# Optimization experiments

Hardware: AMD Instinct MI355X
Metric: run time of the kernel (lower is better)

Reference implementation:

```python
import jax, jax.numpy as jnp
import numpy as np

NUM_HOSTS = 13


def gcn_conv_max(x, src, dst, n, W, b):
    """PyG GCNConv with aggr='max': x@W, gcn_norm (self-loops + sym norm), max-scatter, +bias.
    src/dst already include self-loop edges."""
    xw = x @ W  # [N, out]
    deg = jnp.zeros((n,), xw.dtype).at[dst].add(1.0)
    dinv = jax.lax.rsqrt(deg)  # deg >= 1 thanks to self-loops
    norm = dinv[src] * dinv[dst]  # [E+N]
    msg = norm[:, None] * xw[src]  # [E+N, out] -- the big gather
    agg = jax.ops.segment_max(msg, dst, num_segments=n)
    return agg + b


def self_attn(v, g, aW, ab, fW, fb, gW, gb):
    """SimpleSelfAttention: softmax over feature dim, weighted-sum over nodes, residual global update."""
    att = jax.nn.softmax(v @ aW + ab, axis=-1)  # [B, Nh, h]
    feat = v @ fW + fb                            # [B, Nh, h]
    out = jnp.sum(att * feat, axis=1)             # [B, h]
    g_ = jnp.concatenate([out, g], axis=-1) @ gW + gb
    return g + g_


def setup_inputs() -> dict:
    key = jax.random.key(0)
    ks = jax.random.split(key, 24)
    IN, H1, H2 = 64, 256, 64
    B, NPG = 256, 200
    N = B * NPG
    E = 409600

    x = jax.random.normal(ks[0], (N, IN), jnp.float32)
    host_idx = (jnp.arange(B)[:, None] * NPG + jnp.arange(NUM_HOSTS)[None, :]).reshape(-1).astype(jnp.int32)
    x = x.at[host_idx, 0].set(1.0)  # hosts = x[:,0]==1
    ei = jax.random.randint(ks[1], (2, E), 0, N, dtype=jnp.int64)

    def lin(k, i, o):
        k1, k2 = jax.random.split(k)
        s = 1.0 / np.sqrt(i)
        return (jax.random.uniform(k1, (i, o), jnp.float32, -s, s),
                jax.random.uniform(k2, (o,), jnp.float32, -s, s))

    W1, b1 = lin(ks[2], IN, H1)
    W2, b2 = lin(ks[3], H1, H2)
    # g0: in=IN, h=H1, g=H1 ; g1: in=H1, h=H1 ; g2: in=H2, h=H2
    a0W, a0b = lin(ks[4], IN, H1); f0W, f0b = lin(ks[5], IN, H1); g0W, g0b = lin(ks[6], H1 + H1, H1)
    a1W, a1b = lin(ks[7], H1, H1); f1W, f1b = lin(ks[8], H1, H1); g1W, g1b = lin(ks[9], H1 + H1, H1)
    a2W, a2b = lin(ks[10], H2, H2); f2W, f2b = lin(ks[11], H2, H2); g2W, g2b = lin(ks[12], H2 + H1, H1)
    o1W, o1b = lin(ks[13], H1, H2)
    o2W, o2b = lin(ks[14], H2, 1)

    return dict(x=x, ei=ei, host_idx=host_idx,
                W1=W1, b1=b1, W2=W2, b2=b2,
                a0W=a0W, a0b=a0b, f0W=f0W, f0b=f0b, g0W=g0W, g0b=g0b,
                a1W=a1W, a1b=a1b, f1W=f1W, f1b=f1b, g1W=g1W, g1b=g1b,
                a2W=a2W, a2b=a2b, f2W=f2W, f2b=f2b, g2W=g2W, g2b=g2b,
                o1W=o1W, o1b=o1b, o2W=o2W, o2b=o2b)


def reference(x, ei, host_idx,
              W1, b1, W2, b2,
              a0W, a0b, f0W, f0b, g0W, g0b,
              a1W, a1b, f1W, f1b, g1W, g1b,
              a2W, a2b, f2W, f2b, g2W, g2b,
              o1W, o1b, o2W, o2b):
    n = x.shape[0]
    B = host_idx.shape[0] // NUM_HOSTS
    loops = jnp.arange(n, dtype=ei.dtype)
    src = jnp.concatenate([ei[0], loops])
    dst = jnp.concatenate([ei[1], loops])

    hx = x[host_idx].reshape(B, NUM_HOSTS, -1)
    g = self_attn(hx, jnp.zeros((B, g0b.shape[0]), x.dtype), a0W, a0b, f0W, f0b, g0W, g0b)

    x1 = jax.nn.relu(gcn_conv_max(x, src, dst, n, W1, b1))
    g = self_attn(x1[host_idx].reshape(B, NUM_HOSTS, -1), g, a1W, a1b, f1W, f1b, g1W, g1b)

    x2 = jax.nn.relu(gcn_conv_max(x1, src, dst, n, W2, b2))
    g = self_attn(x2[host_idx].reshape(B, NUM_HOSTS, -1), g, a2W, a2b, f2W, f2b, g2W, g2b)

    return jax.nn.relu(g @ o1W + o1b) @ o2W + o2b  # [B, 1]
```

## Files before the change

### kernel.cpp

```cpp
#include <hip/hip_runtime.h>
#include <math.h>
#include <stdio.h>

#define N_NODES 51200
#define N_EDGES 409600
#define B_GRAPH 256
#define NH 13

typedef float v4f __attribute__((ext_vector_type(4)));
__device__ __forceinline__ void nt_store_f4(float* p, float4 v) {
    v4f w; w.x = v.x; w.y = v.y; w.z = v.z; w.w = v.w;
    __builtin_nontemporal_store(w, (v4f*)p);
}

__device__ __forceinline__ unsigned pack_bf2(float a, float b) {
    unsigned ua = __float_as_uint(a);
    ua = (ua + 0x7fffu + ((ua >> 16) & 1u)) >> 16;
    unsigned ub = __float_as_uint(b);
    ub = (ub + 0x7fffu + ((ub >> 16) & 1u)) & 0xffff0000u;
    return ua | ub;
}
__device__ __forceinline__ float bf_lo(unsigned u) { return __uint_as_float(u << 16); }
__device__ __forceinline__ float bf_hi(unsigned u) { return __uint_as_float(u & 0xffff0000u); }

__device__ __forceinline__ bool ei_is_64(const int* __restrict__ ei32) {
    int z = 1;
    #pragma unroll
    for (int k = 1; k < 16; k += 2) z &= (ei32[k] == 0);
    return z != 0;
}

__global__ void count_deg(const int* __restrict__ ei32, const long long* __restrict__ ei64,
                          int* __restrict__ degc) {
    int e = blockIdx.x * 256 + threadIdx.x;
    if (e >= N_EDGES) return;
    int v = ei_is_64(ei32) ? (int)ei64[N_EDGES + e] : ei32[N_EDGES + e];
    atomicAdd(&degc[v], 1);
}

__global__ void scan_block_sums(const int* __restrict__ degc, int* __restrict__ bsums) {
    __shared__ int sdata[256];
    int i = blockIdx.x * 256 + threadIdx.x;
    sdata[threadIdx.x] = degc[i];
    __syncthreads();
    for (int s = 128; s > 0; s >>= 1) {
        if (threadIdx.x < s) sdata[threadIdx.x] += sdata[threadIdx.x + s];
        __syncthreads();
    }
    if (threadIdx.x == 0) bsums[blockIdx.x] = sdata[0];
}

__global__ void scan_finalize(int* __restrict__ degc, int* __restrict__ offs,
                              float* __restrict__ dinv, const int* __restrict__ bsums) {
    __shared__ int bs[256];
    __shared__ int s[256];
    const int t = threadIdx.x;
    bs[t] = (t < 200) ? bsums[t] : 0;
    __syncthreads();
    for (int off = 1; off < 256; off <<= 1) {
        int u = (t >= off) ? bs[t - off] : 0;
        __syncthreads();
        bs[t] += u;
        __syncthreads();
    }
    int i = blockIdx.x * 256 + t;
    int cnt = degc[i];
    s[t] = cnt;
    __syncthreads();
    for (int off = 1; off < 256; off <<= 1) {
        int u = (t >= off) ? s[t - off] : 0;
        __syncthreads();
        s[t] += u;
        __syncthreads();
    }
    int base = (blockIdx.x == 0) ? 0 : bs[blockIdx.x - 1];
    int excl = base + s[t] - cnt;
    offs[i] = excl;
    dinv[i] = rsqrtf((float)(cnt + 1));
    degc[i] = excl;
    if (i == N_NODES - 1) offs[N_NODES] = N_EDGES;
}

template <int K, int WS, int YS, bool GATHER, bool SCALE, bool BIAS, bool BF16OUT>
__device__ __forceinline__ void gemm_body(const float* __restrict__ X,
        const float* __restrict__ W, const float* __restrict__ bias,
        const float* __restrict__ dinv, float* __restrict__ Y,
        int row0, const int* __restrict__ rows,
        float* __restrict__ xs, float* __restrict__ ws) {
    constexpr int BK = 32;
    constexpr int XS = BK + 4;
    const int t = threadIdx.x;
    const int ct = t & 15;
    const int rt = t >> 4;
    float acc[4][4] = {{0.f}};
    for (int kc = 0; kc < K; kc += BK) {
        __syncthreads();
        #pragma unroll
        for (int i = 0; i < 2; ++i) {
            int idx = t + i * 256;
            int q = idx & 7, r = idx >> 3;
            int xr = GATHER ? rows[r] : (row0 + r);
            float4 v = *(const float4*)(X + (size_t)xr * K + kc + q * 4);
            *(float4*)&xs[r * XS + q * 4] = v;
        }
        #pragma unroll
        for (int i = 0; i < 2; ++i) {
            int idx = t + i * 256;
            int q = idx & 15, k = idx >> 4;
            float4 v = *(const float4*)(W + (size_t)(kc + k) * WS + q * 4);
            *(float4*)&ws[k * 64 + q * 4] = v;
        }
        __syncthreads();
        #pragma unroll
        for (int kb = 0; kb < BK; kb += 4) {
            float4 wv[4];
            #pragma unroll
            for (int kk = 0; kk < 4; ++kk)
                wv[kk] = *(const float4*)&ws[(kb + kk) * 64 + ct * 4];
            #pragma unroll
            for (int r = 0; r < 4; ++r) {
                float4 xv = *(const float4*)&xs[(rt * 4 + r) * XS + kb];
                acc[r][0] = fmaf(xv.x, wv[0].x, acc[r][0]);
                acc[r][1] = fmaf(xv.x, wv[0].y, acc[r][1]);
                acc[r][2] = fmaf(xv.x, wv[0].z, acc[r][2]);
                acc[r][3] = fmaf(xv.x, wv[0].w, acc[r][3]);
                acc[r][0] = fmaf(xv.y, wv[1].x, acc[r][0]);
                acc[r][1] = fmaf(xv.y, wv[1].y, acc[r][1]);
                acc[r][2] = fmaf(xv.y, wv[1].z, acc[r][2]);
                acc[r][3] = fmaf(xv.y, wv[1].w, acc[r][3]);
                acc[r][0] = fmaf(xv.z, wv[2].x, acc[r][0]);
                acc[r][1] = fmaf(xv.z, wv[2].y, acc[r][1]);
                acc[r][2] = fmaf(xv.z, wv[2].z, acc[r][2]);
                acc[r][3] = fmaf(xv.z, wv[2].w, acc[r][3]);
                acc[r][0] = fmaf(xv.w, wv[3].x, acc[r][0]);
                acc[r][1] = fmaf(xv.w, wv[3].y, acc[r][1]);
                acc[r][2] = fmaf(xv.w, wv[3].z, acc[r][2]);
                acc[r][3] = fmaf(xv.w, wv[3].w, acc[r][3]);
            }
        }
    }
    #pragma unroll
    for (int r = 0; r < 4; ++r) {
        int row = row0 + rt * 4 + r;
        float4 o = make_float4(acc[r][0], acc[r][1], acc[r][2], acc[r][3]);
        if (BIAS) {
            o.x += bias[ct * 4 + 0];
            o.y += bias[ct * 4 + 1];
            o.z += bias[ct * 4 + 2];
            o.w += bias[ct * 4 + 3];
        }
        if (SCALE) {
            float sc = dinv[row];
            o.x *= sc; o.y *= sc; o.z *= sc; o.w *= sc;
        }
        if (BF16OUT) {
            unsigned short* yb = (unsigned short*)Y + (size_t)row * YS;
            uint2 pk;
            pk.x = pack_bf2(o.x, o.y);
            pk.y = pack_bf2(o.z, o.w);
            ((uint2*)yb)[ct] = pk;
        } else {
            *(float4*)&Y[(size_t)row * YS + ct * 4] = o;
        }
    }
}

template <int K, int NTOT, int NA_BLK, int NF_BLK, bool BF16Y>
__global__ __launch_bounds__(256) void fused_gemm(const float* __restrict__ X,
        const float* __restrict__ W, float* __restrict__ Y,
        const float* __restrict__ dinv,
        const int* __restrict__ ei32, const long long* __restrict__ ei64,
        int* __restrict__ cursor, int* __restrict__ csr,
        const float* __restrict__ XA, const int* __restrict__ host_idx,
        const float* __restrict__ aW, const float* __restrict__ ab,
        const float* __restrict__ fW, const float* __restrict__ fb,
        float* __restrict__ AF) {
    __shared__ float xs[64 * 36];
    __shared__ float ws[32 * 64];
    __shared__ int rows[64];
    const int bid = blockIdx.x;
    const int t = threadIdx.x;
    if (bid < NA_BLK) {
        const int rb = bid >> 3;
        const int cb = bid & 7;
        const int c0 = cb * 64;
        const float* Wp = (c0 < 256) ? (aW + c0) : (fW + (c0 - 256));
        const float* bp = (c0 < 256) ? (ab + c0) : (fb + (c0 - 256));
        if (t < 64) rows[t] = host_idx[rb * 64 + t];
        gemm_body<K, 256, 512, true, false, true, false>(
            XA, Wp, bp, nullptr, AF + c0, rb * 64, rows, xs, ws);
    } else if (bid < NA_BLK + NF_BLK) {
        int e = (bid - NA_BLK) * 256 + t;
        if (e < N_EDGES) {
            int u, v;
            if (ei_is_64(ei32)) { u = (int)ei64[e]; v = (int)ei64[N_EDGES + e]; }
            else                { u = ei32[e];      v = ei32[N_EDGES + e]; }
            int pos = atomicAdd(&cursor[v], 1);
            csr[pos] = u;
        }
    } else {
        const int gbid = bid - NA_BLK - NF_BLK;
        constexpr int nColBlk = NTOT / 64;
        const int rb = gbid / nColBlk;
        const int cb = gbid - rb * nColBlk;
        float* Yp = BF16Y ? (Y + cb * 32) : (Y + cb * 64);
        gemm_body<K, NTOT, NTOT, false, true, false, BF16Y>(
            X, W + cb * 64, nullptr, dinv, Yp, rb * 64, nullptr, xs, ws);
    }
}

__device__ __forceinline__ void attn_red256(const float* __restrict__ AF,
        const float* __restrict__ gW, const float* __restrict__ gb,
        const float* __restrict__ g_in, float* __restrict__ g_out, int b,
        float (*At)[256], float* red_m, float* red_s, float* cat) {
    const int t = threadIdx.x;
    const int wave = t >> 6, lane = t & 63;
    float accA[NH], accF[NH];
    #pragma unroll
    for (int j = 0; j < NH; ++j) {
        const float* r = AF + (size_t)(b * NH + j) * 512;
        accA[j] = r[t];
        accF[j] = r[256 + t];
        At[j][t] = accA[j];
    }
    __syncthreads();
    for (int j = wave; j < NH; j += 4) {
        float m = -3.402823466e38f;
        #pragma unroll
        for (int q = 0; q < 4; ++q) m = fmaxf(m, At[j][q * 64 + lane]);
        #pragma unroll
        for (int off = 32; off; off >>= 1) m = fmaxf(m, __shfl_xor(m, off));
        if (lane == 0) red_m[j] = m;
    }
    __syncthreads();
    #pragma unroll
    for (int j = 0; j < NH; ++j) At[j][t] = expf(accA[j] - red_m[j]);
    __syncthreads();
    for (int j = wave; j < NH; j += 4) {
        float s = 0.f;
        #pragma unroll
        for (int q = 0; q < 4; ++q) s += At[j][q * 64 + lane];
        #pragma unroll
        for (int off = 32; off; off >>= 1) s += __shfl_xor(s, off);
        if (lane == 0) red_s[j] = s;
    }
    __syncthreads();
    float outc = 0.f;
    #pragma unroll
    for (int j = 0; j < NH; ++j) outc += At[j][t] / red_s[j] * accF[j];
    cat[t] = outc;
    float gv = g_in ? g_in[b * 256 + t] : 0.f;
    cat[256 + t] = gv;
    __syncthreads();
    float acc = gb[t];
    const float* gwp = gW + t;
    #pragma unroll 4
    for (int i4 = 0; i4 < 128; ++i4) {
        float4 cq = ((const float4*)cat)[i4];
        const float* gw4 = gwp + (size_t)i4 * 4 * 256;
        acc = fmaf(cq.x, gw4[0], acc);
        acc = fmaf(cq.y, gw4[256], acc);
        acc = fmaf(cq.z, gw4[512], acc);
        acc = fmaf(cq.w, gw4[768], acc);
    }
    g_out[b * 256 + t] = gv + acc;
}

__global__ __launch_bounds__(256) void fused_agg256(const uint2* __restrict__ xwb,
        const float* __restrict__ dinv, const int* __restrict__ offs,
        const int* __restrict__ csr, const float* __restrict__ bias,
        float* __restrict__ out,
        const float* __restrict__ AF, const float* __restrict__ gW,
        const float* __restrict__ gb, const float* __restrict__ g_in,
        float* __restrict__ g_out) {
    __shared__ float At[NH][256];
    __shared__ float red_m[NH];
    __shared__ float red_s[NH];
    __shared__ float cat[512];
    const int bid = blockIdx.x;
    if (bid < 256) {
        attn_red256(AF, gW, gb, g_in, g_out, bid, At, red_m, red_s, cat);
        return;
    }
    int gid = (bid - 256) * 256 + threadIdx.x;
    int v = gid >> 6;
    int lane = gid & 63;
    uint2 sw = xwb[(size_t)v * 64 + lane];
    float4 acc = make_float4(bf_lo(sw.x), bf_hi(sw.x), bf_lo(sw.y), bf_hi(sw.y));
    int e0 = offs[v];
    int e1 = offs[v + 1];
    int em = e0 + ((e1 - e0) & ~7);
    for (int e = e0; e < em; e += 8) {
        int u[8];
        #pragma unroll
        for (int i = 0; i < 8; ++i) u[i] = csr[e + i];
        uint2 m[8];
        #pragma unroll
        for (int i = 0; i < 8; ++i) m[i] = xwb[(size_t)u[i] * 64 + lane];
        #pragma unroll
        for (int i = 0; i < 8; ++i) {
            acc.x = fmaxf(acc.x, bf_lo(m[i].x));
            acc.y = fmaxf(acc.y, bf_hi(m[i].x));
            acc.z = fmaxf(acc.z, bf_lo(m[i].y));
            acc.w = fmaxf(acc.w, bf_hi(m[i].y));
        }
    }
    if (em < e1) {
        int u[8];
        #pragma unroll
        for (int i = 0; i < 8; ++i) u[i] = csr[(em + i < e1) ? (em + i) : (e1 - 1)];
        uint2 m[8];
        #pragma unroll
        for (int i = 0; i < 8; ++i) m[i] = xwb[(size_t)u[i] * 64 + lane];
        #pragma unroll
        for (int i = 0; i < 8; ++i) {
            if (em + i < e1) {
                acc.x = fmaxf(acc.x, bf_lo(m[i].x));
                acc.y = fmaxf(acc.y, bf_hi(m[i].x));
                acc.z = fmaxf(acc.z, bf_lo(m[i].y));
                acc.w = fmaxf(acc.w, bf_hi(m[i].y));
            }
        }
    }
    float dv = dinv[v];
    float4 b4 = ((const float4*)bias)[lane];
    float4 o;
    o.x = fmaxf(fmaf(acc.x, dv, b4.x), 0.f);
    o.y = fmaxf(fmaf(acc.y, dv, b4.y), 0.f);
    o.z = fmaxf(fmaf(acc.z, dv, b4.z), 0.f);
    o.w = fmaxf(fmaf(acc.w, dv, b4.w), 0.f);
    nt_store_f4(out + (size_t)v * 256 + lane * 4, o);
}

__global__ __launch_bounds__(1024) void attn_graph_head(
        const float* __restrict__ AF,
        const float* __restrict__ g1W, const float* __restrict__ g1b,
        const float* __restrict__ g_in,
        const float* __restrict__ xw2,
        const float* __restrict__ dinv, const int* __restrict__ offs,
        const int* __restrict__ csr, const float* __restrict__ b2,
        const int* __restrict__ host_idx,
        const float* __restrict__ a2W, const float* __restrict__ a2b,
        const float* __restrict__ f2W, const float* __restrict__ f2b,
        const float* __restrict__ g2W, const float* __restrict__ g2b,
        const float* __restrict__ o1W, const float* __restrict__ o1b,
        const float* __restrict__ o2W, const float* __restrict__ o2b,
        float* __restrict__ out) {
    __shared__ float At[NH][256];
    __shared__ float Ft[NH][256];
    __shared__ float red_m[NH];
    __shared__ float red_s[NH];
    __shared__ float cat[512];
    __shared__ float catB[320];
    __shared__ float g1s[256];
    __shared__ float x2l[NH][64];
    __shared__ float part4[4][256];
    __shared__ float part16[16][64];
    __shared__ float grow[256];
    const int b = blockIdx.x;
    const int t = threadIdx.x;
    const int wave = t >> 6;
    const int lane = t & 63;
    const int c = t & 255;
    const int quad = t >> 8;

    if (wave < NH) {
        int hv = host_idx[b * NH + wave];
        float acc = xw2[(size_t)hv * 64 + lane];
        int e0 = offs[hv], e1 = offs[hv + 1];
        for (int e = e0; e < e1; e += 8) {
            int u[8];
            #pragma unroll
            for (int i = 0; i < 8; ++i) u[i] = csr[(e + i < e1) ? (e + i) : (e1 - 1)];
            float m[8];
            #pragma unroll
            for (int i = 0; i < 8; ++i) m[i] = xw2[(size_t)u[i] * 64 + lane];
            #pragma unroll
            for (int i = 0; i < 8; ++i)
                if (e + i < e1) acc = fmaxf(acc, m[i]);
        }
        x2l[wave][lane] = fmaxf(fmaf(acc, dinv[hv], b2[lane]), 0.f);
    }
    for (int idx = t; idx < NH * 128; idx += 1024) {
        int j = idx >> 7, q = idx & 127;
        float4 v = ((const float4*)(AF + (size_t)(b * NH + j) * 512))[q];
        if (q < 64) *(float4*)&At[j][q * 4] = v;
        else        *(float4*)&Ft[j][(q - 64) * 4] = v;
    }
    __syncthreads();
    if (wave < NH) {
        float m = -3.402823466e38f;
        #pragma unroll
        for (int q = 0; q < 4; ++q) m = fmaxf(m, At[wave][q * 64 + lane]);
        #pragma unroll
        for (int off = 32; off; off >>= 1) m = fmaxf(m, __shfl_xor(m, off));
        if (lane == 0) red_m[wave] = m;
    }
    __syncthreads();
    for (int idx = t; idx < NH * 256; idx += 1024) {
        int j = idx >> 8, cc = idx & 255;
        At[j][cc] = expf(At[j][cc] - red_m[j]);
    }
    __syncthreads();
    if (wave < NH) {
        float s = 0.f;
        #pragma unroll
        for (int q = 0; q < 4; ++q) s += At[wave][q * 64 + lane];
        #pragma unroll
        for (int off = 32; off; off >>= 1) s += __shfl_xor(s, off);
        if (lane == 0) red_s[wave] = s;
    }
    __syncthreads();
    if (quad == 0) {
        float outc = 0.f;
        #pragma unroll
        for (int j = 0; j < NH; ++j) outc += At[j][c] / red_s[j] * Ft[j][c];
        cat[c] = outc;
        cat[256 + c] = g_in[b * 256 + c];
    }
    __syncthreads();
    {
        float acc = 0.f;
        const float* gwp = g1W + c;
        #pragma unroll 4
        for (int i4 = quad * 32; i4 < quad * 32 + 32; ++i4) {
            float4 cq = ((const float4*)cat)[i4];
            const float* gw4 = gwp + (size_t)i4 * 1024;
            acc = fmaf(cq.x, gw4[0], acc);
            acc = fmaf(cq.y, gw4[256], acc);
            acc = fmaf(cq.z, gw4[512], acc);
            acc = fmaf(cq.w, gw4[768], acc);
        }
        part4[quad][c] = acc;
    }
    __syncthreads();
    if (quad == 0)
        g1s[c] = cat[256 + c] + g1b[c] +
                 part4[0][c] + part4[1][c] + part4[2][c] + part4[3][c];
    __syncthreads();
    if (wave < NH) {
        float aA = a2b[lane], aF = f2b[lane];
        #pragma unroll 8
        for (int k = 0; k < 64; ++k) {
            float xv = x2l[wave][k];
            aA = fmaf(xv, a2W[k * 64 + lane], aA);
            aF = fmaf(xv, f2W[k * 64 + lane], aF);
        }
        float m = aA;
        #pragma unroll
        for (int off = 32; off; off >>= 1) m = fmaxf(m, __shfl_xor(m, off));
        float pexp = expf(aA - m);
        float s = pexp;
        #pragma unroll
        for (int off = 32; off; off >>= 1) s += __shfl_xor(s, off);
        At[wave][lane] = pexp / s * aF;
    }
    __syncthreads();
    if (t < 64) {
        float o = 0.f;
        #pragma unroll
        for (int j = 0; j < NH; ++j) o += At[j][t];
        catB[t] = o;
    }
    if (quad == 0) catB[64 + c] = g1s[c];
    __syncthreads();
    {
        float acc = 0.f;
        const float* gwp = g2W + c;
        #pragma unroll 4
        for (int i4 = quad * 20; i4 < quad * 20 + 20; ++i4) {
            float4 cq = ((const float4*)catB)[i4];
            const float* gw4 = gwp + (size_t)i4 * 1024;
            acc = fmaf(cq.x, gw4[0], acc);
            acc = fmaf(cq.y, gw4[256], acc);
            acc = fmaf(cq.z, gw4[512], acc);
            acc = fmaf(cq.w, gw4[768], acc);
        }
        part4[quad][c] = acc;
    }
    __syncthreads();
    if (quad == 0)
        grow[c] = g1s[c] + g2b[c] +
                  part4[0][c] + part4[1][c] + part4[2][c] + part4[3][c];
    __syncthreads();
    {
        float hp = 0.f;
        #pragma unroll
        for (int k = wave * 16; k < wave * 16 + 16; ++k)
            hp = fmaf(grow[k], o1W[(size_t)k * 64 + lane], hp);
        part16[wave][lane] = hp;
    }
    __syncthreads();
    if (wave == 0) {
        float h = o1b[lane];
        #pragma unroll
        for (int w = 0; w < 16; ++w) h += part16[w][lane];
        h = fmaxf(h, 0.f);
        float sres = h * o2W[lane];
        #pragma unroll
        for (int off = 32; off; off >>= 1) sres += __shfl_xor(sres, off);
        if (lane == 0) out[b] = sres + o2b[0];
    }
}

extern "C" void kernel_launch(void* const* d_in, const int* in_sizes, int n_in,
                              void* d_out, int out_size, void* d_ws, size_t ws_size,
                              hipStream_t stream) {
    (void)in_sizes; (void)n_in; (void)out_size;
    const float* x    = (const float*)d_in[0];
    const int* ei32   = (const int*)d_in[1];
    const long long* ei64 = (const long long*)d_in[1];
    const int* hidx   = (const int*)d_in[2];
    const float* W1 = (const float*)d_in[3],  *b1 = (const float*)d_in[4];
    const float* W2 = (const float*)d_in[5],  *b2 = (const float*)d_in[6];
    const float* a0W = (const float*)d_in[7],  *a0b = (const float*)d_in[8];
    const float* f0W = (const float*)d_in[9],  *f0b = (const float*)d_in[10];
    const float* g0W = (const float*)d_in[11], *g0b = (const float*)d_in[12];
    const float* a1W = (const float*)d_in[13], *a1b = (const float*)d_in[14];
    const float* f1W = (const float*)d_in[15], *f1b = (const float*)d_in[16];
    const float* g1W = (const float*)d_in[17], *g1b = (const float*)d_in[18];
    const float* a2W = (const float*)d_in[19], *a2b = (const float*)d_in[20];
    const float* f2W = (const float*)d_in[21], *f2b = (const float*)d_in[22];
    const float* g2W = (const float*)d_in[23], *g2b = (const float*)d_in[24];
    const float* o1W = (const float*)d_in[25], *o1b = (const float*)d_in[26];
    const float* o2W = (const float*)d_in[27], *o2b = (const float*)d_in[28];
    float* outp = (float*)d_out;

    char* p = (char*)d_ws;
    auto alloc = [&](size_t bytes) {
        char* r = p;
        p += (bytes + 255) & ~(size_t)255;
        return r;
    };
    float* dinv = (float*)alloc((size_t)N_NODES * 4);
    int* degc   = (int*)alloc((size_t)N_NODES * 4);
    int* offs   = (int*)alloc((size_t)(N_NODES + 1) * 4);
    int* csr    = (int*)alloc((size_t)N_EDGES * 4);
    int* bsums  = (int*)alloc(256 * 4);
    float* g    = (float*)alloc((size_t)B_GRAPH * 256 * 4);
    float* AF   = (float*)alloc((size_t)B_GRAPH * NH * 512 * 4);
    unsigned short* xw1b = (unsigned short*)alloc((size_t)N_NODES * 256 * 2);
    float* x1   = (float*)alloc((size_t)N_NODES * 256 * 4);
    float* xw2  = (float*)alloc((size_t)N_NODES * 64 * 4);

    size_t need = (size_t)(p - (char*)d_ws);
    if (need > ws_size) {
        fprintf(stderr, "kernel_launch: ws too small (%zu needed, %zu have)\n", need, ws_size);
        return;
    }

    (void)hipMemsetAsync(degc, 0, (size_t)N_NODES * 4, stream);
    count_deg<<<1600, 256, 0, stream>>>(ei32, ei64, degc);
    scan_block_sums<<<200, 256, 0, stream>>>(degc, bsums);
    scan_finalize<<<200, 256, 0, stream>>>(degc, offs, dinv, bsums);

    fused_gemm<64, 256, 416, 1600, true><<<416 + 1600 + 3200, 256, 0, stream>>>(
        x, W1, (float*)xw1b, dinv, ei32, ei64, degc, csr,
        x, hidx, a0W, a0b, f0W, f0b, AF);
    fused_agg256<<<256 + 12800, 256, 0, stream>>>((const uint2*)xw1b, dinv, offs, csr,
                                                  b1, x1, AF, g0W, g0b, nullptr, g);
    fused_gemm<256, 64, 416, 0, false><<<416 + 800, 256, 0, stream>>>(
        x1, W2, xw2, dinv, ei32, ei64, degc, csr,
        x1, hidx, a1W, a1b, f1W, f1b, AF);
    attn_graph_head<<<256, 1024, 0, stream>>>(
        AF, g1W, g1b, g, xw2, dinv, offs, csr, b2, hidx,
        a2W, a2b, f2W, f2b, g2W, g2b, o1W, o1b, o2W, o2b, outp);
}
```

Baseline: 301.2 us.

## Store layer-1 activations in bf16 and enlarge GEMM register tiles

The aggregation kernel now writes x1 as packed bf16 instead of fp32, which halves the write and the later read traffic for the 51200x256 activation. The second GEMM and the host-attention GEMM read it back by unpacking bf16 into shared memory. The main node GEMMs move to 128-row tiles with 8 rows per thread (8 or 4 columns), raising register-level reuse and cutting the number of blocks. The extra rounding of x1 to bf16 adds precision loss, and the larger per-thread accumulators raise register pressure.

```diff
diff --git a/kernel.cpp b/kernel.cpp
--- a/kernel.cpp
+++ b/kernel.cpp
@@ -8,9 +8,10 @@
 #define NH 13
 
 typedef float v4f __attribute__((ext_vector_type(4)));
-__device__ __forceinline__ void nt_store_f4(float* p, float4 v) {
-    v4f w; w.x = v.x; w.y = v.y; w.z = v.z; w.w = v.w;
-    __builtin_nontemporal_store(w, (v4f*)p);
+typedef unsigned v2u __attribute__((ext_vector_type(2)));
+__device__ __forceinline__ void nt_store_u2(uint2* p, uint2 v) {
+    v2u w; w.x = v.x; w.y = v.y;
+    __builtin_nontemporal_store(w, (v2u*)p);
 }
 
 __device__ __forceinline__ unsigned pack_bf2(float a, float b) {
@@ -81,11 +82,10 @@
     if (i == N_NODES - 1) offs[N_NODES] = N_EDGES;
 }
 
-template <int K, int WS, int YS, bool GATHER, bool SCALE, bool BIAS, bool BF16OUT>
-__device__ __forceinline__ void gemm_body(const float* __restrict__ X,
+template <int K, int WS, bool BF16IN>
+__device__ __forceinline__ void gemm_body64(const float* __restrict__ X,
         const float* __restrict__ W, const float* __restrict__ bias,
-        const float* __restrict__ dinv, float* __restrict__ Y,
-        int row0, const int* __restrict__ rows,
+        float* __restrict__ Y, int row0, const int* __restrict__ rows,
         float* __restrict__ xs, float* __restrict__ ws) {
     constexpr int BK = 32;
     constexpr int XS = BK + 4;
@@ -99,8 +99,14 @@
         for (int i = 0; i < 2; ++i) {
             int idx = t + i * 256;
             int q = idx & 7, r = idx >> 3;
-            int xr = GATHER ? rows[r] : (row0 + r);
-            float4 v = *(const float4*)(X + (size_t)xr * K + kc + q * 4);
+            int xr = rows[r];
+            float4 v;
+            if (BF16IN) {
+                uint2 pv = ((const uint2*)X)[(size_t)xr * (K / 4) + kc / 4 + q];
+                v = make_float4(bf_lo(pv.x), bf_hi(pv.x), bf_lo(pv.y), bf_hi(pv.y));
+            } else {
+                v = *(const float4*)(X + (size_t)xr * K + kc + q * 4);
+            }
             *(float4*)&xs[r * XS + q * 4] = v;
         }
         #pragma unroll
@@ -120,77 +126,137 @@
             #pragma unroll
             for (int r = 0; r < 4; ++r) {
                 float4 xv = *(const float4*)&xs[(rt * 4 + r) * XS + kb];
-                acc[r][0] = fmaf(xv.x, wv[0].x, acc[r][0]);
-                acc[r][1] = fmaf(xv.x, wv[0].y, acc[r][1]);
-                acc[r][2] = fmaf(xv.x, wv[0].z, acc[r][2]);
-                acc[r][3] = fmaf(xv.x, wv[0].w, acc[r][3]);
-                acc[r][0] = fmaf(xv.y, wv[1].x, acc[r][0]);
-                acc[r][1] = fmaf(xv.y, wv[1].y, acc[r][1]);
-                acc[r][2] = fmaf(xv.y, wv[1].z, acc[r][2]);
-                acc[r][3] = fmaf(xv.y, wv[1].w, acc[r][3]);
-                acc[r][0] = fmaf(xv.z, wv[2].x, acc[r][0]);
-                acc[r][1] = fmaf(xv.z, wv[2].y, acc[r][1]);
-                acc[r][2] = fmaf(xv.z, wv[2].z, acc[r][2]);
-                acc[r][3] = fmaf(xv.z, wv[2].w, acc[r][3]);
-                acc[r][0] = fmaf(xv.w, wv[3].x, acc[r][0]);
-                acc[r][1] = fmaf(xv.w, wv[3].y, acc[r][1]);
-                acc[r][2] = fmaf(xv.w, wv[3].z, acc[r][2]);
-                acc[r][3] = fmaf(xv.w, wv[3].w, acc[r][3]);
+                float xk[4] = {xv.x, xv.y, xv.z, xv.w};
+                #pragma unroll
+                for (int kk = 0; kk < 4; ++kk) {
+                    acc[r][0] = fmaf(xk[kk], wv[kk].x, acc[r][0]);
+                    acc[r][1] = fmaf(xk[kk], wv[kk].y, acc[r][1]);
+                    acc[r][2] = fmaf(xk[kk], wv[kk].z, acc[r][2]);
+                    acc[r][3] = fmaf(xk[kk], wv[kk].w, acc[r][3]);
+                }
             }
         }
     }
     #pragma unroll
     for (int r = 0; r < 4; ++r) {
         int row = row0 + rt * 4 + r;
-        float4 o = make_float4(acc[r][0], acc[r][1], acc[r][2], acc[r][3]);
-        if (BIAS) {
-            o.x += bias[ct * 4 + 0];
-            o.y += bias[ct * 4 + 1];
-            o.z += bias[ct * 4 + 2];
-            o.w += bias[ct * 4 + 3];
-        }
-        if (SCALE) {
-            float sc = dinv[row];
-            o.x *= sc; o.y *= sc; o.z *= sc; o.w *= sc;
-        }
-        if (BF16OUT) {
-            unsigned short* yb = (unsigned short*)Y + (size_t)row * YS;
-            uint2 pk;
-            pk.x = pack_bf2(o.x, o.y);
-            pk.y = pack_bf2(o.z, o.w);
-            ((uint2*)yb)[ct] = pk;
-        } else {
-            *(float4*)&Y[(size_t)row * YS + ct * 4] = o;
-        }
-    }
-}
-
-template <int K, int NTOT, int NA_BLK, int NF_BLK, bool BF16Y>
-__global__ __launch_bounds__(256) void fused_gemm(const float* __restrict__ X,
-        const float* __restrict__ W, float* __restrict__ Y,
+        float4 o = make_float4(acc[r][0] + bias[ct * 4 + 0],
+                               acc[r][1] + bias[ct * 4 + 1],
+                               acc[r][2] + bias[ct * 4 + 2],
+                               acc[r][3] + bias[ct * 4 + 3]);
+        *(float4*)&Y[(size_t)row * 512 + ct * 4] = o;
+    }
+}
+
+template <int K, int WS, int YS, int NCOLB, int CPT, bool BF16IN, bool BF16OUT>
+__device__ __forceinline__ void gemm_main(const float* __restrict__ X,
+        const float* __restrict__ W, const float* __restrict__ dinv,
+        float* __restrict__ Y, int row0,
+        float* __restrict__ xs, float* __restrict__ ws) {
+    constexpr int BK = 32;
+    constexpr int XS = BK + 4;
+    constexpr int CQ = CPT / 4;
+    const int t = threadIdx.x;
+    const int ct = t & 15;
+    const int rt = t >> 4;
+    float acc[8][CPT];
+    #pragma unroll
+    for (int r = 0; r < 8; ++r)
+        #pragma unroll
+        for (int c = 0; c < CPT; ++c) acc[r][c] = 0.f;
+    for (int kc = 0; kc < K; kc += BK) {
+        __syncthreads();
+        #pragma unroll
+        for (int i = 0; i < 4; ++i) {
+            int idx = t + i * 256;
+            int q = idx & 7, r = idx >> 3;
+            float4 v;
+            if (BF16IN) {
+                uint2 pv = ((const uint2*)X)[(size_t)(row0 + r) * (K / 4) + kc / 4 + q];
+                v = make_float4(bf_lo(pv.x), bf_hi(pv.x), bf_lo(pv.y), bf_hi(pv.y));
+            } else {
+                v = *(const float4*)(X + (size_t)(row0 + r) * K + kc + q * 4);
+            }
+            *(float4*)&xs[r * XS + q * 4] = v;
+        }
+        #pragma unroll
+        for (int i = 0; i < NCOLB / 32; ++i) {
+            int idx = t + i * 256;
+            int q = idx & (NCOLB / 4 - 1), k = idx / (NCOLB / 4);
+            float4 v = *(const float4*)(W + (size_t)(kc + k) * WS + q * 4);
+            *(float4*)&ws[k * NCOLB + q * 4] = v;
+        }
+        __syncthreads();
+        #pragma unroll
+        for (int kb = 0; kb < BK; kb += 4) {
+            float4 wv[4][CQ];
+            #pragma unroll
+            for (int kk = 0; kk < 4; ++kk)
+                #pragma unroll
+                for (int cq = 0; cq < CQ; ++cq)
+                    wv[kk][cq] = *(const float4*)&ws[(kb + kk) * NCOLB + ct * CPT + cq * 4];
+            #pragma unroll
+            for (int r = 0; r < 8; ++r) {
+                float4 xv = *(const float4*)&xs[(rt * 8 + r) * XS + kb];
+                float xk[4] = {xv.x, xv.y, xv.z, xv.w};
+                #pragma unroll
+                for (int kk = 0; kk < 4; ++kk)
+                    #pragma unroll
+                    for (int cq = 0; cq < CQ; ++cq) {
+                        acc[r][cq * 4 + 0] = fmaf(xk[kk], wv[kk][cq].x, acc[r][cq * 4 + 0]);
+                        acc[r][cq * 4 + 1] = fmaf(xk[kk], wv[kk][cq].y, acc[r][cq * 4 + 1]);
+                        acc[r][cq * 4 + 2] = fmaf(xk[kk], wv[kk][cq].z, acc[r][cq * 4 + 2]);
+                        acc[r][cq * 4 + 3] = fmaf(xk[kk], wv[kk][cq].w, acc[r][cq * 4 + 3]);
+                    }
+            }
+        }
+    }
+    #pragma unroll
+    for (int r = 0; r < 8; ++r) {
+        int row = row0 + rt * 8 + r;
+        float sc = dinv[row];
+        #pragma unroll
+        for (int cq = 0; cq < CQ; ++cq) {
+            float4 o = make_float4(acc[r][cq * 4 + 0] * sc, acc[r][cq * 4 + 1] * sc,
+                                   acc[r][cq * 4 + 2] * sc, acc[r][cq * 4 + 3] * sc);
+            if (BF16OUT) {
+                unsigned short* yb = (unsigned short*)Y + (size_t)row * YS;
+                uint2 pk;
+                pk.x = pack_bf2(o.x, o.y);
+                pk.y = pack_bf2(o.z, o.w);
+                ((uint2*)yb)[ct * CQ + cq] = pk;
+            } else {
+                *(float4*)&Y[(size_t)row * YS + ct * CPT + cq * 4] = o;
+            }
+        }
+    }
+}
+
+__global__ __launch_bounds__(256) void fused_gemm1(const float* __restrict__ x,
+        const float* __restrict__ W1, float* __restrict__ xw1b,
         const float* __restrict__ dinv,
         const int* __restrict__ ei32, const long long* __restrict__ ei64,
         int* __restrict__ cursor, int* __restrict__ csr,
-        const float* __restrict__ XA, const int* __restrict__ host_idx,
-        const float* __restrict__ aW, const float* __restrict__ ab,
-        const float* __restrict__ fW, const float* __restrict__ fb,
+        const int* __restrict__ host_idx,
+        const float* __restrict__ a0W, const float* __restrict__ a0b,
+        const float* __restrict__ f0W, const float* __restrict__ f0b,
         float* __restrict__ AF) {
-    __shared__ float xs[64 * 36];
-    __shared__ float ws[32 * 64];
+    __shared__ float xs[128 * 36];
+    __shared__ float ws[32 * 128];
     __shared__ int rows[64];
     const int bid = blockIdx.x;
     const int t = threadIdx.x;
-    if (bid < NA_BLK) {
+    if (bid < 416) {
         const int rb = bid >> 3;
         const int cb = bid & 7;
         const int c0 = cb * 64;
-        const float* Wp = (c0 < 256) ? (aW + c0) : (fW + (c0 - 256));
-        const float* bp = (c0 < 256) ? (ab + c0) : (fb + (c0 - 256));
+        const float* Wp = (c0 < 256) ? (a0W + c0) : (f0W + (c0 - 256));
+        const float* bp = (c0 < 256) ? (a0b + c0) : (f0b + (c0 - 256));
         if (t < 64) rows[t] = host_idx[rb * 64 + t];
-        gemm_body<K, 256, 512, true, false, true, false>(
-            XA, Wp, bp, nullptr, AF + c0, rb * 64, rows, xs, ws);
-    } else if (bid < NA_BLK + NF_BLK) {
-        int e = (bid - NA_BLK) * 256 + t;
+        __syncthreads();
+        gemm_body64<64, 256, false>(x, Wp, bp, AF + c0, rb * 64, rows, xs, ws);
+    } else if (bid < 2016) {
+        int e = (bid - 416) * 256 + t;
         if (e < N_EDGES) {
             int u, v;
             if (ei_is_64(ei32)) { u = (int)ei64[e]; v = (int)ei64[N_EDGES + e]; }
@@ -199,13 +265,39 @@
             csr[pos] = u;
         }
     } else {
-        const int gbid = bid - NA_BLK - NF_BLK;
-        constexpr int nColBlk = NTOT / 64;
-        const int rb = gbid / nColBlk;
-        const int cb = gbid - rb * nColBlk;
-        float* Yp = BF16Y ? (Y + cb * 32) : (Y + cb * 64);
-        gemm_body<K, NTOT, NTOT, false, true, false, BF16Y>(
-            X, W + cb * 64, nullptr, dinv, Yp, rb * 64, nullptr, xs, ws);
+        const int gbid = bid - 2016;
+        const int rb = gbid >> 1;
+        const int cb = gbid & 1;
+        gemm_main<64, 256, 256, 128, 8, false, true>(
+            x, W1 + cb * 128, dinv, xw1b + cb * 64, rb * 128, xs, ws);
+    }
+}
+
+__global__ __launch_bounds__(256) void fused_gemm2(const float* __restrict__ x1b,
+        const float* __restrict__ W2, float* __restrict__ xw2,
+        const float* __restrict__ dinv,
+        const int* __restrict__ host_idx,
+        const float* __restrict__ a1W, const float* __restrict__ a1b,
+        const float* __restrict__ f1W, const float* __restrict__ f1b,
+        float* __restrict__ AF) {
+    __shared__ float xs[128 * 36];
+    __shared__ float ws[32 * 64];
+    __shared__ int rows[64];
+    const int bid = blockIdx.x;
+    const int t = threadIdx.x;
+    if (bid < 416) {
+        const int rb = bid >> 3;
+        const int cb = bid & 7;
+        const int c0 = cb * 64;
+        const float* Wp = (c0 < 256) ? (a1W + c0) : (f1W + (c0 - 256));
+        const float* bp = (c0 < 256) ? (a1b + c0) : (f1b + (c0 - 256));
+        if (t < 64) rows[t] = host_idx[rb * 64 + t];
+        __syncthreads();
+        gemm_body64<256, 256, true>(x1b, Wp, bp, AF + c0, rb * 64, rows, xs, ws);
+    } else {
+        const int gbid = bid - 416;
+        gemm_main<256, 64, 64, 64, 4, true, false>(
+            x1b, W2, dinv, xw2, gbid * 128, xs, ws);
     }
 }
 
@@ -269,7 +361,7 @@
 __global__ __launch_bounds__(256) void fused_agg256(const uint2* __restrict__ xwb,
         const float* __restrict__ dinv, const int* __restrict__ offs,
         const int* __restrict__ csr, const float* __restrict__ bias,
-        float* __restrict__ out,
+        uint2* __restrict__ outb,
         const float* __restrict__ AF, const float* __restrict__ gW,
         const float* __restrict__ gb, const float* __restrict__ g_in,
         float* __restrict__ g_out) {
@@ -329,7 +421,10 @@
     o.y = fmaxf(fmaf(acc.y, dv, b4.y), 0.f);
     o.z = fmaxf(fmaf(acc.z, dv, b4.z), 0.f);
     o.w = fmaxf(fmaf(acc.w, dv, b4.w), 0.f);
-    nt_store_f4(out + (size_t)v * 256 + lane * 4, o);
+    uint2 pk;
+    pk.x = pack_bf2(o.x, o.y);
+    pk.y = pack_bf2(o.z, o.w);
+    nt_store_u2(outb + (size_t)v * 64 + lane, pk);
 }
 
 __global__ __launch_bounds__(1024) void attn_graph_head(
@@ -540,7 +635,7 @@
     float* g    = (float*)alloc((size_t)B_GRAPH * 256 * 4);
     float* AF   = (float*)alloc((size_t)B_GRAPH * NH * 512 * 4);
     unsigned short* xw1b = (unsigned short*)alloc((size_t)N_NODES * 256 * 2);
-    float* x1   = (float*)alloc((size_t)N_NODES * 256 * 4);
+    unsigned short* x1b  = (unsigned short*)alloc((size_t)N_NODES * 256 * 2);
     float* xw2  = (float*)alloc((size_t)N_NODES * 64 * 4);
 
     size_t need = (size_t)(p - (char*)d_ws);
@@ -554,14 +649,14 @@
     scan_block_sums<<<200, 256, 0, stream>>>(degc, bsums);
     scan_finalize<<<200, 256, 0, stream>>>(degc, offs, dinv, bsums);
 
-    fused_gemm<64, 256, 416, 1600, true><<<416 + 1600 + 3200, 256, 0, stream>>>(
+    fused_gemm1<<<2816, 256, 0, stream>>>(
         x, W1, (float*)xw1b, dinv, ei32, ei64, degc, csr,
-        x, hidx, a0W, a0b, f0W, f0b, AF);
+        hidx, a0W, a0b, f0W, f0b, AF);
     fused_agg256<<<256 + 12800, 256, 0, stream>>>((const uint2*)xw1b, dinv, offs, csr,
-                                                  b1, x1, AF, g0W, g0b, nullptr, g);
-    fused_gemm<256, 64, 416, 0, false><<<416 + 800, 256, 0, stream>>>(
-        x1, W2, xw2, dinv, ei32, ei64, degc, csr,
-        x1, hidx, a1W, a1b, f1W, f1b, AF);
+                                                  b1, (uint2*)x1b, AF, g0W, g0b,
+                                                  nullptr, g);
+    fused_gemm2<<<816, 256, 0, stream>>>(
+        (const float*)x1b, W2, xw2, dinv, hidx, a1W, a1b, f1W, f1b, AF);
     attn_graph_head<<<256, 1024, 0, stream>>>(
         AF, g1W, g1b, g, xw2, dinv, offs, csr, b2, hidx,
         a2W, a2b, f2W, f2b, g2W, g2b, o1W, o1b, o2W, o2b, outp);
```

Result: no change. 297.3 us (-1.3%).
